# Performance work log

Measured on AMD Instinct MI355X. Metric: run time of the kernel, lower is better.

## Reference

```python
import jax, jax.numpy as jnp
import numpy as np

B, T, D = 8, 4096, 256
INNER, S = D * 2, 16          # expand=2, d_state=16
CODEBOOK, THRESH = 240, 0.7


def setup_inputs() -> dict:
    key = jax.random.key(0)
    ks = iter(jax.random.split(key, 32))
    nrm = lambda shape, s=0.02: jax.random.normal(next(ks), shape, dtype=jnp.float32) * s
    return {
        'x': jax.random.normal(next(ks), (B, T, D), dtype=jnp.float32),
        # Mamba backend params
        'in_proj_w': nrm((D, 2 * INNER)), 'in_proj_b': jnp.zeros((2 * INNER,), jnp.float32),
        'conv_proj_w': nrm((INNER, INNER)), 'conv_proj_b': jnp.zeros((INNER,), jnp.float32),
        'A_log': jax.random.normal(next(ks), (INNER, S), dtype=jnp.float32) * 0.01,
        'bc_proj_w': nrm((INNER, 2 * S)), 'bc_proj_b': jnp.zeros((2 * S,), jnp.float32),
        'dt_proj_w': nrm((INNER, INNER)), 'dt_proj_b': jnp.zeros((INNER,), jnp.float32),
        'out_proj_w': nrm((INNER, D)), 'out_proj_b': jnp.zeros((D,), jnp.float32),
        # CatastropheDetector params
        'cat1_w': nrm((D, 64)), 'cat1_b': jnp.zeros((64,), jnp.float32),
        'cat2_w': nrm((64, 32)), 'cat2_b': jnp.zeros((32,), jnp.float32),
        'risk_w': nrm((32, 1)), 'risk_b': jnp.zeros((1,), jnp.float32),
        # E8 quantizer params
        'e8a_w': nrm((D, 64)), 'e8a_b': jnp.zeros((64,), jnp.float32),
        'e8b_w': nrm((64, 8)), 'e8b_b': jnp.zeros((8,), jnp.float32),
        'e8_codebook': jax.random.normal(next(ks), (CODEBOOK, 8), dtype=jnp.float32) * 0.1,
    }


def reference(x, in_proj_w, in_proj_b, conv_proj_w, conv_proj_b, A_log,
              bc_proj_w, bc_proj_b, dt_proj_w, dt_proj_b, out_proj_w, out_proj_b,
              cat1_w, cat1_b, cat2_w, cat2_b, risk_w, risk_b,
              e8a_w, e8a_b, e8b_w, e8b_b, e8_codebook):
    # ---- Mamba selective-scan dynamics ----
    xp = x @ in_proj_w + in_proj_b                       # [B,T,2*inner]
    x_main, x_gate = jnp.split(xp, 2, axis=-1)
    x_conv = jax.nn.silu(x_main @ conv_proj_w + conv_proj_b)  # [B,T,inner]
    A = -jnp.exp(A_log)                                  # [inner,S]
    bc = x_conv @ bc_proj_w + bc_proj_b                  # [B,T,2S]
    Bp, Cp = jnp.split(bc, 2, axis=-1)                   # [B,T,S] each
    dt = jax.nn.softplus(x_conv @ dt_proj_w + dt_proj_b) # [B,T,inner]

    def step(h, ins):  # h: [B,inner,S]
        x_t, dt_t, B_t, C_t = ins                        # [B,inner],[B,inner],[B,S],[B,S]
        A_bar = jnp.exp(dt_t[..., None] * A)
        h = A_bar * h + (dt_t[..., None] * B_t[:, None, :]) * x_t[..., None]
        y_t = (h * C_t[:, None, :]).sum(-1)              # [B,inner]
        return h, y_t

    h0 = jnp.zeros((x.shape[0], A_log.shape[0], A_log.shape[1]), x.dtype)
    xs = (x_conv.transpose(1, 0, 2), dt.transpose(1, 0, 2),
          Bp.transpose(1, 0, 2), Cp.transpose(1, 0, 2))
    _, y = jax.lax.scan(step, h0, xs)                    # [T,B,inner]
    y = y.transpose(1, 0, 2) * jax.nn.silu(x_gate)
    y = y @ out_proj_w + out_proj_b                      # [B,T,D]

    # ---- Catastrophe / bifurcation detector ----
    f = jax.nn.gelu(y @ cat1_w + cat1_b)
    f = f @ cat2_w + cat2_b
    risk = jax.nn.sigmoid((f @ risk_w + risk_b).squeeze(-1))  # [B,T]
    vel = jnp.diff(y, axis=1, prepend=y[:, :1])
    vn = jnp.linalg.norm(vel, axis=-1)                   # [B,T]
    acc = jnp.abs(jnp.diff(vn, axis=1, prepend=vn[:, :1]))
    combined = 0.5 * risk + 0.3 * jax.nn.sigmoid(vn) + 0.2 * jax.nn.sigmoid(acc)
    is_bif = combined > THRESH

    # ---- E8 quantization with straight-through estimator ----
    e8c = jax.nn.gelu(y @ e8a_w + e8a_b) @ e8b_w + e8b_b # [B,T,8]
    flat = e8c.reshape(-1, 8)
    d2 = ((flat ** 2).sum(1, keepdims=True)
          - 2.0 * flat @ e8_codebook.T
          + (e8_codebook ** 2).sum(1)[None, :])          # [B*T,240]
    idx = jnp.argmin(d2, axis=1)
    q = e8_codebook[idx].reshape(e8c.shape)
    e8_codes = e8c + jax.lax.stop_gradient(q - e8c)
    return (y, e8_codes, idx.reshape(y.shape[0], y.shape[1]), is_bif)
```

## Files before the change

### kernel.cpp

```cpp
#include <hip/hip_runtime.h>
#include <hip/hip_bf16.h>
#include <math.h>

#define BB 8
#define TT 4096
#define DD 256
#define INNER 512
#define SS 16
#define MTOK (BB*TT)
#define NCODE 240

#define SCAN_NC 64
#define SCAN_L  64

typedef unsigned short u16;
typedef unsigned int   u32;
typedef __attribute__((ext_vector_type(8))) short short8;
typedef __attribute__((ext_vector_type(4))) float f32x4;

__device__ __forceinline__ float sigmoidf_(float x) { return 1.f / (1.f + expf(-x)); }
__device__ __forceinline__ float siluf_(float x)    { return x / (1.f + expf(-x)); }
__device__ __forceinline__ float geluf_(float x) {
    float x3 = x * x * x;
    return 0.5f * x * (1.f + tanhf(0.7978845608028654f * (x + 0.044715f * x3)));
}
__device__ __forceinline__ float softplusf_(float x) {
    return fmaxf(x, 0.f) + log1pf(expf(-fabsf(x)));
}

__device__ __forceinline__ u16 f2bf(float v) {
    u32 u = __float_as_uint(v);
    u32 r = (u + 0x7FFFu + ((u >> 16) & 1u)) >> 16;
    return (u16)r;
}
__device__ __forceinline__ float bf2f(u16 h) {
    return __uint_as_float(((u32)h) << 16);
}

__device__ __forceinline__ void gload16(const void* g, void* l) {
    __builtin_amdgcn_global_load_lds((const __attribute__((address_space(1))) u32*)g,
                                     (__attribute__((address_space(3))) u32*)l, 16, 0, 0);
}

template<int MODE, int CT>
__global__ __launch_bounds__(256)
void gemmS(const u16* __restrict__ Ah, const u16* __restrict__ Al, int K,
           const u16* __restrict__ BTh, const u16* __restrict__ BTl,
           const float* __restrict__ bias,
           float* __restrict__ out0, float* __restrict__ out1,
           u16* __restrict__ oh, u16* __restrict__ ol)
{
    __shared__ u16 sm[4][128 * 32];

    const int tid  = threadIdx.x;
    const int lane = tid & 63;
    const int wv   = tid >> 6;
    const int wr   = wv >> 1;
    const int wc   = wv & 1;
    const int lc   = lane & 15;
    const int kc   = lane >> 4;

    const int i    = blockIdx.x;
    const int xcd  = i & 7;
    const int j    = i >> 3;
    const int row0 = (xcd * 32 + j / CT) * 128;
    const int col0 = (j % CT) * 128;

    const u16* Agh = Ah + (size_t)row0 * K;
    const u16* Agl = Al + (size_t)row0 * K;
    const u16* Bgh = BTh + (size_t)col0 * K;
    const u16* Bgl = BTl + (size_t)col0 * K;

    f32x4 acc[4][4];
    #pragma unroll
    for (int m = 0; m < 4; ++m)
        #pragma unroll
        for (int n = 0; n < 4; ++n) acc[m][n] = (f32x4)0.f;

    for (int k0 = 0; k0 < K; k0 += 32) {
        #pragma unroll
        for (int c = 0; c < 2; ++c) {
            int e = c * 256 + tid;
            int row = e >> 2, ch = e & 3;
            int chs = ch ^ ((row >> 1) & 3);
            size_t go = (size_t)row * K + k0 + chs * 8;
            gload16(Agh + go, &sm[0][e * 8]);
            gload16(Agl + go, &sm[1][e * 8]);
            gload16(Bgh + go, &sm[2][e * 8]);
            gload16(Bgl + go, &sm[3][e * 8]);
        }
        __syncthreads();

        short8 ah[4], al[4], bh[4], bl[4];
        #pragma unroll
        for (int m = 0; m < 4; ++m) {
            int row = wr * 64 + m * 16 + lc;
            int off = row * 32 + ((kc ^ ((row >> 1) & 3)) << 3);
            ah[m] = *(const short8*)&sm[0][off];
            al[m] = *(const short8*)&sm[1][off];
        }
        #pragma unroll
        for (int n = 0; n < 4; ++n) {
            int row = wc * 64 + n * 16 + lc;
            int off = row * 32 + ((kc ^ ((row >> 1) & 3)) << 3);
            bh[n] = *(const short8*)&sm[2][off];
            bl[n] = *(const short8*)&sm[3][off];
        }
        #pragma unroll
        for (int m = 0; m < 4; ++m)
            #pragma unroll
            for (int n = 0; n < 4; ++n) {
                acc[m][n] = __builtin_amdgcn_mfma_f32_16x16x32_bf16(ah[m], bh[n], acc[m][n], 0, 0, 0);
                acc[m][n] = __builtin_amdgcn_mfma_f32_16x16x32_bf16(ah[m], bl[n], acc[m][n], 0, 0, 0);
                acc[m][n] = __builtin_amdgcn_mfma_f32_16x16x32_bf16(al[m], bh[n], acc[m][n], 0, 0, 0);
            }
        __syncthreads();
    }

    #pragma unroll
    for (int n = 0; n < 4; ++n) {
        int colg = col0 + wc * 64 + n * 16 + lc;
        float bv = bias[colg];
        #pragma unroll
        for (int m = 0; m < 4; ++m) {
            f32x4 a = acc[m][n];
            #pragma unroll
            for (int r = 0; r < 4; ++r) {
                int rowg = row0 + wr * 64 + m * 16 + kc * 4 + r;
                float v = a[r] + bv;
                if (MODE == 0) {
                    if (colg < 512) {
                        u16 hh = f2bf(v);
                        oh[(size_t)rowg * 512 + colg] = hh;
                        ol[(size_t)rowg * 512 + colg] = f2bf(v - bf2f(hh));
                    } else {
                        out0[(size_t)rowg * 512 + colg - 512] = v;
                    }
                } else if (MODE == 1) {
                    v = siluf_(v);
                    u16 hh = f2bf(v);
                    oh[(size_t)rowg * 512 + colg] = hh;
                    ol[(size_t)rowg * 512 + colg] = f2bf(v - bf2f(hh));
                } else if (MODE == 2) {
                    if (colg < 512) {
                        out0[(size_t)rowg * 512 + colg] = softplusf_(v);
                    } else if (colg < 544) {
                        out1[(size_t)rowg * 32 + colg - 512] = v;
                    }
                } else if (MODE == 4) {
                    out0[(size_t)rowg * 256 + colg] = v;
                    u16 hh = f2bf(v);
                    oh[(size_t)rowg * 256 + colg] = hh;
                    ol[(size_t)rowg * 256 + colg] = f2bf(v - bf2f(hh));
                } else {
                    out0[(size_t)rowg * 128 + colg] = geluf_(v);
                }
            }
        }
    }
}

__global__ __launch_bounds__(256)
void split_kernel(const float* __restrict__ s, u16* __restrict__ h,
                  u16* __restrict__ l, int n)
{
    int i = blockIdx.x * 256 + threadIdx.x;
    if (i >= n) return;
    float v = s[i];
    u16 hh = f2bf(v);
    h[i] = hh;
    l[i] = f2bf(v - bf2f(hh));
}

__global__ __launch_bounds__(256)
void prep_weights(const float* __restrict__ in_proj_w, const float* __restrict__ conv_w,
                  const float* __restrict__ dt_w, const float* __restrict__ bc_w,
                  const float* __restrict__ out_w,
                  const float* __restrict__ cat1_w, const float* __restrict__ e8a_w,
                  const float* __restrict__ dt_b, const float* __restrict__ bc_b,
                  const float* __restrict__ cat1_b, const float* __restrict__ e8a_b,
                  u16* __restrict__ wiTh, u16* __restrict__ wiTl,
                  u16* __restrict__ wcTh, u16* __restrict__ wcTl,
                  u16* __restrict__ wdbTh, u16* __restrict__ wdbTl,
                  u16* __restrict__ woTh, u16* __restrict__ woTl,
                  u16* __restrict__ whTh, u16* __restrict__ whTl,
                  float* __restrict__ dbbias, float* __restrict__ hbias)
{
    int idx = blockIdx.x * 256 + threadIdx.x;
    float v; u16 *dh, *dl; int off;
    if (idx < 262144) {
        int e = idx, n = e >> 8, k = e & 255;
        v = in_proj_w[(size_t)k * 1024 + n]; dh = wiTh; dl = wiTl; off = e;
    } else if (idx < 524288) {
        int e = idx - 262144, n = e >> 9, k = e & 511;
        v = conv_w[(size_t)k * 512 + n]; dh = wcTh; dl = wcTl; off = e;
    } else if (idx < 851968) {
        int e = idx - 524288, n = e >> 9, k = e & 511;
        v = (n < 512) ? dt_w[(size_t)k * 512 + n]
                      : ((n < 544) ? bc_w[(size_t)k * 32 + (n - 512)] : 0.f);
        dh = wdbTh; dl = wdbTl; off = e;
    } else if (idx < 983040) {
        int e = idx - 851968, n = e >> 9, k = e & 511;
        v = out_w[(size_t)k * 256 + n]; dh = woTh; dl = woTl; off = e;
    } else if (idx < 1015808) {
        int e = idx - 983040, n = e >> 8, k = e & 255;
        v = (n < 64) ? cat1_w[(size_t)k * 64 + n] : e8a_w[(size_t)k * 64 + (n - 64)];
        dh = whTh; dl = whTl; off = e;
    } else if (idx < 1015808 + 640) {
        int i = idx - 1015808;
        dbbias[i] = (i < 512) ? dt_b[i] : ((i < 544) ? bc_b[i - 512] : 0.f);
        return;
    } else if (idx < 1015808 + 640 + 128) {
        int i = idx - 1015808 - 640;
        hbias[i] = (i < 64) ? cat1_b[i] : e8a_b[i - 64];
        return;
    } else return;
    u16 hh = f2bf(v); dh[off] = hh; dl[off] = f2bf(v - bf2f(hh));
}

__global__ __launch_bounds__(256)
void scan_pass1(const float* __restrict__ DT, const u16* __restrict__ XCh,
                const u16* __restrict__ XCl, const float* __restrict__ BC,
                const float* __restrict__ A_log,
                float* __restrict__ Pbuf, float* __restrict__ Hbuf)
{
    const int bid  = blockIdx.x;
    const int half = bid & 1;
    const int c    = (bid >> 1) & (SCAN_NC - 1);
    const int b    = bid >> 7;
    const int ch   = half * 256 + threadIdx.x;
    const int row0 = b * TT + c * SCAN_L;

    float A[16];
    {
        const float4* ar = (const float4*)(A_log + ch * 16);
        #pragma unroll
        for (int q = 0; q < 4; ++q) {
            float4 v = ar[q];
            A[q * 4 + 0] = -__expf(v.x);
            A[q * 4 + 1] = -__expf(v.y);
            A[q * 4 + 2] = -__expf(v.z);
            A[q * 4 + 3] = -__expf(v.w);
        }
    }

    float h[16];
    #pragma unroll
    for (int s = 0; s < 16; ++s) h[s] = 0.f;
    float dtsum = 0.f;

    const float* dtp = DT  + (size_t)row0 * 512 + ch;
    const u16*   xhp = XCh + (size_t)row0 * 512 + ch;
    const u16*   xlp = XCl + (size_t)row0 * 512 + ch;
    const float* bcp = BC  + (size_t)row0 * 32;

    float dv = dtp[0];
    float xv = bf2f(xhp[0]) + bf2f(xlp[0]);
    for (int t = 0; t < SCAN_L; ++t) {
        const int tn = (t + 1 < SCAN_L) ? t + 1 : t;
        float dvn = dtp[(size_t)tn * 512];
        float xvn = bf2f(xhp[(size_t)tn * 512]) + bf2f(xlp[(size_t)tn * 512]);
        const float* br = bcp + (size_t)t * 32;
        float dtx = dv * xv;
        dtsum += dv;
        #pragma unroll
        for (int s = 0; s < 16; ++s) {
            float a = __expf(dv * A[s]);
            h[s] = fmaf(a, h[s], dtx * br[s]);
        }
        dv = dvn; xv = xvn;
    }

    size_t o = ((size_t)(b * SCAN_NC + c) * 512 + ch) * 16;
    #pragma unroll
    for (int s = 0; s < 16; ++s) {
        Pbuf[o + s] = __expf(dtsum * A[s]);
        Hbuf[o + s] = h[s];
    }
}

__global__ __launch_bounds__(256)
void scan_pass2(const float* __restrict__ Pbuf, float* __restrict__ Hbuf)
{
    const int idx = blockIdx.x * 256 + threadIdx.x;
    const int b = idx >> 13;
    const int ds = idx & 8191;
    float hin = 0.f;
    for (int c = 0; c < SCAN_NC; ++c) {
        size_t o = ((size_t)(b * SCAN_NC + c)) * (INNER * SS) + ds;
        float p = Pbuf[o], hh = Hbuf[o];
        Hbuf[o] = hin;
        hin = fmaf(p, hin, hh);
    }
}

__global__ __launch_bounds__(256)
void scan_pass3(const float* __restrict__ DT, const u16* __restrict__ XCh,
                const u16* __restrict__ XCl, const float* __restrict__ BC,
                const float* __restrict__ A_log, const float* __restrict__ GATE,
                const float* __restrict__ Hin,
                u16* __restrict__ YGh, u16* __restrict__ YGl)
{
    const int bid  = blockIdx.x;
    const int half = bid & 1;
    const int c    = (bid >> 1) & (SCAN_NC - 1);
    const int b    = bid >> 7;
    const int ch   = half * 256 + threadIdx.x;
    const int row0 = b * TT + c * SCAN_L;

    float A[16];
    {
        const float4* ar = (const float4*)(A_log + ch * 16);
        #pragma unroll
        for (int q = 0; q < 4; ++q) {
            float4 v = ar[q];
            A[q * 4 + 0] = -__expf(v.x);
            A[q * 4 + 1] = -__expf(v.y);
            A[q * 4 + 2] = -__expf(v.z);
            A[q * 4 + 3] = -__expf(v.w);
        }
    }

    float h[16];
    {
        size_t o = ((size_t)(b * SCAN_NC + c) * 512 + ch) * 16;
        const float4* hr = (const float4*)(Hin + o);
        #pragma unroll
        for (int q = 0; q < 4; ++q) {
            float4 v = hr[q];
            h[q * 4 + 0] = v.x; h[q * 4 + 1] = v.y;
            h[q * 4 + 2] = v.z; h[q * 4 + 3] = v.w;
        }
    }

    const float* dtp = DT   + (size_t)row0 * 512 + ch;
    const u16*   xhp = XCh  + (size_t)row0 * 512 + ch;
    const u16*   xlp = XCl  + (size_t)row0 * 512 + ch;
    const float* gtp = GATE + (size_t)row0 * 512 + ch;
    const float* bcp = BC   + (size_t)row0 * 32;
    u16* yhp = YGh + (size_t)row0 * 512 + ch;
    u16* ylp = YGl + (size_t)row0 * 512 + ch;

    float dv = dtp[0];
    float xv = bf2f(xhp[0]) + bf2f(xlp[0]);
    float gv = gtp[0];
    for (int t = 0; t < SCAN_L; ++t) {
        const int tn = (t + 1 < SCAN_L) ? t + 1 : t;
        float dvn = dtp[(size_t)tn * 512];
        float xvn = bf2f(xhp[(size_t)tn * 512]) + bf2f(xlp[(size_t)tn * 512]);
        float gvn = gtp[(size_t)tn * 512];
        const float* br = bcp + (size_t)t * 32;
        float dtx = dv * xv;
        float y = 0.f;
        #pragma unroll
        for (int s = 0; s < 16; ++s) {
            float a = __expf(dv * A[s]);
            h[s] = fmaf(a, h[s], dtx * br[s]);
            y = fmaf(h[s], br[16 + s], y);
        }
        float yg = y * siluf_(gv);
        u16 hh = f2bf(yg);
        yhp[(size_t)t * 512] = hh;
        ylp[(size_t)t * 512] = f2bf(yg - bf2f(hh));
        dv = dvn; xv = xvn; gv = gvn;
    }
}

__global__ __launch_bounds__(256)
void head_finish(const float* __restrict__ F1,
                 const float* __restrict__ w2, const float* __restrict__ b2,
                 const float* __restrict__ w3, const float* __restrict__ b3,
                 const float* __restrict__ wb, const float* __restrict__ bb,
                 const float* __restrict__ cb,
                 float* __restrict__ risk, float* __restrict__ codes_out,
                 float* __restrict__ idx_out)
{
    __shared__ float F1s[64][129];
    __shared__ float w2S[64 * 32];
    __shared__ float wbS[64 * 8];
    __shared__ float cbS[NCODE * 8];
    __shared__ float cnS[NCODE];
    __shared__ float w3S[32];
    __shared__ float b2S[32];
    __shared__ float bbS[8];
    const int tid = threadIdx.x;
    const int tok0 = blockIdx.x * 64;

    for (int e = tid; e < 64 * 128; e += 256)
        F1s[e >> 7][e & 127] = F1[(size_t)tok0 * 128 + e];
    for (int e = tid; e < 64 * 32; e += 256) w2S[e] = w2[e];
    for (int e = tid; e < 64 * 8; e += 256) wbS[e] = wb[e];
    for (int e = tid; e < NCODE * 8; e += 256) cbS[e] = cb[e];
    if (tid < 32) { w3S[tid] = w3[tid]; b2S[tid] = b2[tid]; }
    if (tid < 8) bbS[tid] = bb[tid];
    __syncthreads();
    for (int e = tid; e < NCODE; e += 256) {
        float s = 0.f;
        #pragma unroll
        for (int q = 0; q < 8; ++q) s = fmaf(cbS[e * 8 + q], cbS[e * 8 + q], s);
        cnS[e] = s;
    }
    __syncthreads();

    const int lane = tid & 63;
    const int wv   = tid >> 6;
    const int tl   = wv * 16 + (lane >> 2);
    const int role = lane & 3;
    const float* f1c = &F1s[tl][0];
    const float* f1e = &F1s[tl][64];

    float v = 0.f;
    float bd = 3.4e38f;
    int bi = 0;

    if (role < 2) {
        float f2[16];
        #pragma unroll
        for (int d = 0; d < 16; ++d) f2[d] = b2S[role * 16 + d];
        for (int k = 0; k < 64; ++k) {
            float fv = f1c[k];
            #pragma unroll
            for (int d = 0; d < 16; ++d)
                f2[d] = fmaf(fv, w2S[k * 32 + role * 16 + d], f2[d]);
        }
        #pragma unroll
        for (int d = 0; d < 16; ++d) v = fmaf(f2[d], w3S[role * 16 + d], v);
    } else {
        float ec[8];
        #pragma unroll
        for (int q = 0; q < 8; ++q) ec[q] = bbS[q];
        for (int k = 0; k < 64; ++k) {
            float fv = f1e[k];
            #pragma unroll
            for (int q = 0; q < 8; ++q) ec[q] = fmaf(fv, wbS[k * 8 + q], ec[q]);
        }
        float fn = 0.f;
        #pragma unroll
        for (int q = 0; q < 8; ++q) fn = fmaf(ec[q], ec[q], fn);
        const int base = (role - 2) * 120;
        for (int i = 0; i < 120; ++i) {
            int cc = base + i;
            float dot = 0.f;
            #pragma unroll
            for (int q = 0; q < 8; ++q) dot = fmaf(ec[q], cbS[cc * 8 + q], dot);
            float d = fn + cnS[cc] - 2.f * dot;
            if (d < bd) { bd = d; bi = cc; }
        }
    }

    float vp = __shfl_xor(v, 1, 64);
    float od = __shfl_xor(bd, 1, 64);
    int   oi = __shfl_xor(bi, 1, 64);
    const int tok = tok0 + tl;
    if (role == 0) risk[tok] = sigmoidf_(v + vp + b3[0]);
    if (role == 2) {
        if (od < bd || (od == bd && oi < bi)) { bd = od; bi = oi; }
        idx_out[tok] = (float)bi;
        #pragma unroll
        for (int q = 0; q < 8; ++q)
            codes_out[(size_t)tok * 8 + q] = cbS[bi * 8 + q];
    }
}

__global__ __launch_bounds__(256)
void vn_kernel(const float* __restrict__ y, float* __restrict__ vn)
{
    const int tid = threadIdx.x;
    const int w = tid >> 6, j = tid & 63;
    const int t = blockIdx.x * 4 + w;
    const int tt = t & (TT - 1);
    const float4* cur = (const float4*)(y + (size_t)t * 256);
    const float4* prv = (const float4*)(y + (size_t)(tt == 0 ? t : t - 1) * 256);
    float4 a = cur[j], b = prv[j];
    float dx = a.x - b.x, dy = a.y - b.y, dz = a.z - b.z, dw = a.w - b.w;
    float ss = dx * dx + dy * dy + dz * dz + dw * dw;
    ss += __shfl_xor(ss, 1, 64);
    ss += __shfl_xor(ss, 2, 64);
    ss += __shfl_xor(ss, 4, 64);
    ss += __shfl_xor(ss, 8, 64);
    ss += __shfl_xor(ss, 16, 64);
    ss += __shfl_xor(ss, 32, 64);
    if (j == 0) vn[t] = sqrtf(ss);
}

__global__ __launch_bounds__(256)
void combined_kernel(const float* __restrict__ risk, const float* __restrict__ vn,
                     float* __restrict__ bif)
{
    const int t = blockIdx.x * 256 + threadIdx.x;
    const int tt = t & (TT - 1);
    float v = vn[t];
    float a = (tt == 0) ? 0.f : fabsf(v - vn[t - 1]);
    float cmb = 0.5f * risk[t] + 0.3f * sigmoidf_(v) + 0.2f * sigmoidf_(a);
    bif[t] = (cmb > 0.7f) ? 1.f : 0.f;
}

extern "C" void kernel_launch(void* const* d_in, const int* in_sizes, int n_in,
                              void* d_out, int out_size, void* d_ws, size_t ws_size,
                              hipStream_t stream)
{
    const float* x          = (const float*)d_in[0];
    const float* in_proj_w  = (const float*)d_in[1];
    const float* in_proj_b  = (const float*)d_in[2];
    const float* conv_w     = (const float*)d_in[3];
    const float* conv_b     = (const float*)d_in[4];
    const float* A_log      = (const float*)d_in[5];
    const float* bc_w       = (const float*)d_in[6];
    const float* bc_b       = (const float*)d_in[7];
    const float* dt_w       = (const float*)d_in[8];
    const float* dt_b       = (const float*)d_in[9];
    const float* out_w      = (const float*)d_in[10];
    const float* out_b      = (const float*)d_in[11];
    const float* cat1_w     = (const float*)d_in[12];
    const float* cat1_b     = (const float*)d_in[13];
    const float* cat2_w     = (const float*)d_in[14];
    const float* cat2_b     = (const float*)d_in[15];
    const float* risk_w     = (const float*)d_in[16];
    const float* risk_b     = (const float*)d_in[17];
    const float* e8a_w      = (const float*)d_in[18];
    const float* e8a_b      = (const float*)d_in[19];
    const float* e8b_w      = (const float*)d_in[20];
    const float* e8b_b      = (const float*)d_in[21];
    const float* codebook   = (const float*)d_in[22];

    float* out = (float*)d_out;
    float* y_out     = out;
    float* codes_out = out + (size_t)MTOK * 256;
    float* idx_out   = codes_out + (size_t)MTOK * 8;
    float* bif_out   = idx_out + MTOK;

    const size_t AL = 255;
    #define ALN(x) (((x) + AL) & ~AL)
    char* p = (char*)d_ws;
    #define TAKE(T, name, bytes) T* name = (T*)p; p += ALN((size_t)(bytes));
    TAKE(float, risk, MTOK * 4)
    TAKE(float, vn,   MTOK * 4)
    TAKE(u16, wiTh, (size_t)1024 * 256 * 2)
    TAKE(u16, wiTl, (size_t)1024 * 256 * 2)
    TAKE(u16, wcTh, (size_t)512 * 512 * 2)
    TAKE(u16, wcTl, (size_t)512 * 512 * 2)
    TAKE(u16, wdbTh, (size_t)640 * 512 * 2)
    TAKE(u16, wdbTl, (size_t)640 * 512 * 2)
    TAKE(u16, woTh, (size_t)256 * 512 * 2)
    TAKE(u16, woTl, (size_t)256 * 512 * 2)
    TAKE(u16, whTh, (size_t)128 * 256 * 2)
    TAKE(u16, whTl, (size_t)128 * 256 * 2)
    TAKE(float, dbbias, 640 * 4)
    TAKE(float, hbias, 128 * 4)
    TAKE(u16, A0, (size_t)2 * MTOK * 512 * 2)
    TAKE(u16, B0, (size_t)2 * MTOK * 512 * 2)
    TAKE(float, GATE, (size_t)MTOK * 512 * 4)
    TAKE(float, BC, (size_t)MTOK * 32 * 4)

    u16* MAINh = A0;
    u16* MAINl = A0 + (size_t)MTOK * 512;
    float* DT  = (float*)A0;
    u16* yh    = A0;
    u16* yl    = A0 + (size_t)MTOK * 512;
    u16* xh  = B0;
    u16* xl  = B0 + (size_t)MTOK * 512;
    u16* XCh = B0;
    u16* XCl = B0 + (size_t)MTOK * 512;
    float* F1 = GATE;
    float* Pb = y_out;
    float* Hb = y_out + (size_t)MTOK * 128;

    split_kernel<<<(MTOK * 256 + 255) / 256, 256, 0, stream>>>(x, xh, xl, MTOK * 256);
    prep_weights<<<(1016576 + 255) / 256, 256, 0, stream>>>(
        in_proj_w, conv_w, dt_w, bc_w, out_w, cat1_w, e8a_w,
        dt_b, bc_b, cat1_b, e8a_b,
        wiTh, wiTl, wcTh, wcTl, wdbTh, wdbTl, woTh, woTl, whTh, whTl,
        dbbias, hbias);

    gemmS<0, 8><<<256 * 8, 256, 0, stream>>>(
        xh, xl, 256, wiTh, wiTl, in_proj_b, GATE, nullptr, MAINh, MAINl);
    gemmS<1, 4><<<256 * 4, 256, 0, stream>>>(
        MAINh, MAINl, 512, wcTh, wcTl, conv_b, nullptr, nullptr, XCh, XCl);
    gemmS<2, 5><<<256 * 5, 256, 0, stream>>>(
        XCh, XCl, 512, wdbTh, wdbTl, dbbias, DT, BC, nullptr, nullptr);
    scan_pass1<<<BB * SCAN_NC * 2, 256, 0, stream>>>(DT, XCh, XCl, BC, A_log, Pb, Hb);
    scan_pass2<<<256, 256, 0, stream>>>(Pb, Hb);
    scan_pass3<<<BB * SCAN_NC * 2, 256, 0, stream>>>(DT, XCh, XCl, BC, A_log, GATE,
                                                     Hb, XCh, XCl);
    gemmS<4, 2><<<256 * 2, 256, 0, stream>>>(
        XCh, XCl, 512, woTh, woTl, out_b, y_out, nullptr, yh, yl);
    gemmS<5, 1><<<256 * 1, 256, 0, stream>>>(
        yh, yl, 256, whTh, whTl, hbias, F1, nullptr, nullptr, nullptr);
    head_finish<<<MTOK / 64, 256, 0, stream>>>(F1, cat2_w, cat2_b, risk_w, risk_b,
                                               e8b_w, e8b_b, codebook,
                                               risk, codes_out, idx_out);
    vn_kernel<<<MTOK / 4, 256, 0, stream>>>(y_out, vn);
    combined_kernel<<<MTOK / 256, 256, 0, stream>>>(risk, vn, bif_out);
}
```

Measured before the change: 722.7 us.

## Fold conv_proj into in_proj by precomputing the combined weight product

Since x_main feeds linearly into conv_proj, the two matmuls are merged: a small kernel computes W_in_main @ W_conv and the folded bias, and the first GEMM applies silu directly, removing the separate 32K x 512 x 512 conv GEMM and its intermediate buffer traffic. The weight product is computed in fp32 each call by small extra kernels. Rounding differs slightly because the intermediate x_main is no longer materialised.

After: 890.4 us. 23.2% more time.

```diff
diff --git a/kernel.cpp b/kernel.cpp
--- a/kernel.cpp
+++ b/kernel.cpp
@@ -130,17 +130,13 @@
                 float v = a[r] + bv;
                 if (MODE == 0) {
                     if (colg < 512) {
+                        v = siluf_(v);
                         u16 hh = f2bf(v);
                         oh[(size_t)rowg * 512 + colg] = hh;
                         ol[(size_t)rowg * 512 + colg] = f2bf(v - bf2f(hh));
                     } else {
                         out0[(size_t)rowg * 512 + colg - 512] = v;
                     }
-                } else if (MODE == 1) {
-                    v = siluf_(v);
-                    u16 hh = f2bf(v);
-                    oh[(size_t)rowg * 512 + colg] = hh;
-                    ol[(size_t)rowg * 512 + colg] = f2bf(v - bf2f(hh));
                 } else if (MODE == 2) {
                     if (colg < 512) {
                         out0[(size_t)rowg * 512 + colg] = softplusf_(v);
@@ -173,14 +169,13 @@
 }
 
 __global__ __launch_bounds__(256)
-void prep_weights(const float* __restrict__ in_proj_w, const float* __restrict__ conv_w,
+void prep_weights(const float* __restrict__ in_proj_w,
                   const float* __restrict__ dt_w, const float* __restrict__ bc_w,
                   const float* __restrict__ out_w,
                   const float* __restrict__ cat1_w, const float* __restrict__ e8a_w,
                   const float* __restrict__ dt_b, const float* __restrict__ bc_b,
                   const float* __restrict__ cat1_b, const float* __restrict__ e8a_b,
                   u16* __restrict__ wiTh, u16* __restrict__ wiTl,
-                  u16* __restrict__ wcTh, u16* __restrict__ wcTl,
                   u16* __restrict__ wdbTh, u16* __restrict__ wdbTl,
                   u16* __restrict__ woTh, u16* __restrict__ woTl,
                   u16* __restrict__ whTh, u16* __restrict__ whTl,
@@ -188,34 +183,97 @@
 {
     int idx = blockIdx.x * 256 + threadIdx.x;
     float v; u16 *dh, *dl; int off;
-    if (idx < 262144) {
-        int e = idx, n = e >> 8, k = e & 255;
-        v = in_proj_w[(size_t)k * 1024 + n]; dh = wiTh; dl = wiTl; off = e;
-    } else if (idx < 524288) {
-        int e = idx - 262144, n = e >> 9, k = e & 511;
-        v = conv_w[(size_t)k * 512 + n]; dh = wcTh; dl = wcTl; off = e;
-    } else if (idx < 851968) {
-        int e = idx - 524288, n = e >> 9, k = e & 511;
+    if (idx < 131072) {
+        int e = idx, n = 512 + (e >> 8), k = e & 255;
+        v = in_proj_w[(size_t)k * 1024 + n]; dh = wiTh; dl = wiTl; off = n * 256 + k;
+    } else if (idx < 458752) {
+        int e = idx - 131072, n = e >> 9, k = e & 511;
         v = (n < 512) ? dt_w[(size_t)k * 512 + n]
                       : ((n < 544) ? bc_w[(size_t)k * 32 + (n - 512)] : 0.f);
         dh = wdbTh; dl = wdbTl; off = e;
-    } else if (idx < 983040) {
-        int e = idx - 851968, n = e >> 9, k = e & 511;
+    } else if (idx < 589824) {
+        int e = idx - 458752, n = e >> 9, k = e & 511;
         v = out_w[(size_t)k * 256 + n]; dh = woTh; dl = woTl; off = e;
-    } else if (idx < 1015808) {
-        int e = idx - 983040, n = e >> 8, k = e & 255;
+    } else if (idx < 622592) {
+        int e = idx - 589824, n = e >> 8, k = e & 255;
         v = (n < 64) ? cat1_w[(size_t)k * 64 + n] : e8a_w[(size_t)k * 64 + (n - 64)];
         dh = whTh; dl = whTl; off = e;
-    } else if (idx < 1015808 + 640) {
-        int i = idx - 1015808;
+    } else if (idx < 622592 + 640) {
+        int i = idx - 622592;
         dbbias[i] = (i < 512) ? dt_b[i] : ((i < 544) ? bc_b[i - 512] : 0.f);
         return;
-    } else if (idx < 1015808 + 640 + 128) {
-        int i = idx - 1015808 - 640;
+    } else if (idx < 622592 + 640 + 128) {
+        int i = idx - 622592 - 640;
         hbias[i] = (i < 64) ? cat1_b[i] : e8a_b[i - 64];
         return;
     } else return;
     u16 hh = f2bf(v); dh[off] = hh; dl[off] = f2bf(v - bf2f(hh));
+}
+
+__global__ __launch_bounds__(256)
+void wprod_kernel(const float* __restrict__ in_proj_w, const float* __restrict__ conv_w,
+                  u16* __restrict__ wiTh, u16* __restrict__ wiTl)
+{
+    __shared__ float As[16][64];
+    __shared__ float Bs[16][65];
+    const int tid = threadIdx.x;
+    const int tx = tid & 15, ty = tid >> 4;
+    const int m0 = blockIdx.y * 64;
+    const int n0 = blockIdx.x * 64;
+    float acc[4][4] = {};
+    for (int j0 = 0; j0 < 512; j0 += 16) {
+        #pragma unroll
+        for (int i = 0; i < 4; ++i) {
+            int e = tid + i * 256;
+            int m = e >> 4, jj = e & 15;
+            As[jj][m] = in_proj_w[(size_t)(m0 + m) * 1024 + j0 + jj];
+            int n = e & 63, j2 = e >> 6;
+            Bs[j2][n] = conv_w[(size_t)(j0 + j2) * 512 + n0 + n];
+        }
+        __syncthreads();
+        #pragma unroll
+        for (int jj = 0; jj < 16; ++jj) {
+            float av[4], bv[4];
+            #pragma unroll
+            for (int i = 0; i < 4; ++i) av[i] = As[jj][ty * 4 + i];
+            #pragma unroll
+            for (int l = 0; l < 4; ++l) bv[l] = Bs[jj][tx * 4 + l];
+            #pragma unroll
+            for (int i = 0; i < 4; ++i)
+                #pragma unroll
+                for (int l = 0; l < 4; ++l)
+                    acc[i][l] = fmaf(av[i], bv[l], acc[i][l]);
+        }
+        __syncthreads();
+    }
+    #pragma unroll
+    for (int i = 0; i < 4; ++i) {
+        int k = m0 + ty * 4 + i;
+        #pragma unroll
+        for (int l = 0; l < 4; ++l) {
+            int n = n0 + tx * 4 + l;
+            float v = acc[i][l];
+            u16 hh = f2bf(v);
+            wiTh[(size_t)n * 256 + k] = hh;
+            wiTl[(size_t)n * 256 + k] = f2bf(v - bf2f(hh));
+        }
+    }
+}
+
+__global__ __launch_bounds__(256)
+void wbias_kernel(const float* __restrict__ in_proj_b, const float* __restrict__ conv_w,
+                  const float* __restrict__ conv_b, float* __restrict__ fbias)
+{
+    int n = blockIdx.x * 256 + threadIdx.x;
+    if (n >= 1024) return;
+    if (n < 512) {
+        float s = conv_b[n];
+        for (int j = 0; j < 512; ++j)
+            s = fmaf(in_proj_b[j], conv_w[(size_t)j * 512 + n], s);
+        fbias[n] = s;
+    } else {
+        fbias[n] = in_proj_b[n];
+    }
 }
 
 __global__ __launch_bounds__(256)
@@ -537,8 +595,6 @@
     TAKE(float, vn,   MTOK * 4)
     TAKE(u16, wiTh, (size_t)1024 * 256 * 2)
     TAKE(u16, wiTl, (size_t)1024 * 256 * 2)
-    TAKE(u16, wcTh, (size_t)512 * 512 * 2)
-    TAKE(u16, wcTl, (size_t)512 * 512 * 2)
     TAKE(u16, wdbTh, (size_t)640 * 512 * 2)
     TAKE(u16, wdbTl, (size_t)640 * 512 * 2)
     TAKE(u16, woTh, (size_t)256 * 512 * 2)
@@ -547,35 +603,34 @@
     TAKE(u16, whTl, (size_t)128 * 256 * 2)
     TAKE(float, dbbias, 640 * 4)
     TAKE(float, hbias, 128 * 4)
+    TAKE(float, fbias, 1024 * 4)
     TAKE(u16, A0, (size_t)2 * MTOK * 512 * 2)
     TAKE(u16, B0, (size_t)2 * MTOK * 512 * 2)
     TAKE(float, GATE, (size_t)MTOK * 512 * 4)
     TAKE(float, BC, (size_t)MTOK * 32 * 4)
 
-    u16* MAINh = A0;
-    u16* MAINl = A0 + (size_t)MTOK * 512;
-    float* DT  = (float*)A0;
-    u16* yh    = A0;
-    u16* yl    = A0 + (size_t)MTOK * 512;
+    u16* XCh = A0;
+    u16* XCl = A0 + (size_t)MTOK * 512;
     u16* xh  = B0;
     u16* xl  = B0 + (size_t)MTOK * 512;
-    u16* XCh = B0;
-    u16* XCl = B0 + (size_t)MTOK * 512;
+    float* DT = (float*)B0;
+    u16* yh   = B0;
+    u16* yl   = B0 + (size_t)MTOK * 512;
     float* F1 = GATE;
     float* Pb = y_out;
     float* Hb = y_out + (size_t)MTOK * 128;
 
     split_kernel<<<(MTOK * 256 + 255) / 256, 256, 0, stream>>>(x, xh, xl, MTOK * 256);
-    prep_weights<<<(1016576 + 255) / 256, 256, 0, stream>>>(
-        in_proj_w, conv_w, dt_w, bc_w, out_w, cat1_w, e8a_w,
+    prep_weights<<<(623360 + 255) / 256, 256, 0, stream>>>(
+        in_proj_w, dt_w, bc_w, out_w, cat1_w, e8a_w,
         dt_b, bc_b, cat1_b, e8a_b,
-        wiTh, wiTl, wcTh, wcTl, wdbTh, wdbTl, woTh, woTl, whTh, whTl,
+        wiTh, wiTl, wdbTh, wdbTl, woTh, woTl, whTh, whTl,
         dbbias, hbias);
+    wprod_kernel<<<dim3(8, 4), 256, 0, stream>>>(in_proj_w, conv_w, wiTh, wiTl);
+    wbias_kernel<<<4, 256, 0, stream>>>(in_proj_b, conv_w, conv_b, fbias);
 
     gemmS<0, 8><<<256 * 8, 256, 0, stream>>>(
-        xh, xl, 256, wiTh, wiTl, in_proj_b, GATE, nullptr, MAINh, MAINl);
-    gemmS<1, 4><<<256 * 4, 256, 0, stream>>>(
-        MAINh, MAINl, 512, wcTh, wcTl, conv_b, nullptr, nullptr, XCh, XCl);
+        xh, xl, 256, wiTh, wiTl, fbias, GATE, nullptr, XCh, XCl);
     gemmS<2, 5><<<256 * 5, 256, 0, stream>>>(
         XCh, XCl, 512, wdbTh, wdbTl, dbbias, DT, BC, nullptr, nullptr);
     scan_pass1<<<BB * SCAN_NC * 2, 256, 0, stream>>>(DT, XCh, XCl, BC, A_log, Pb, Hb);
```
